# Optimization experiments

Hardware: AMD Instinct MI355X
Metric: run time of the kernel (lower is better)

Reference implementation:

```python
import jax, jax.numpy as jnp
import numpy as np

H = 1024        # hidden_dim
MD = 2048       # memory_dim
L = 16384       # memory length == max_length
N = 8           # head_N
# sys.float_info.min underflows to 0.0 in float32, exactly as in the torch
# original (python float * float32 tensor). Kept for faithfulness.
TINY = jnp.float32(2.2250738585072014e-308)


def setup_inputs() -> dict:
    key = jax.random.key(0)
    ks = jax.random.split(key, 12)
    s_h = 1.0 / np.sqrt(H)
    s_m = 1.0 / np.sqrt(MD)
    s_o = 1.0 / np.sqrt(2 * H)
    return {
        "x": jax.random.normal(ks[0], (1, 1, H), jnp.float32),
        "memory": jax.random.normal(ks[1], (L, MD), jnp.float32),
        "Wq": jax.random.uniform(ks[2], (H, H), jnp.float32, -s_h, s_h),
        "bq": jax.random.uniform(ks[3], (H,), jnp.float32, -s_h, s_h),
        "Wk": jax.random.uniform(ks[4], (H, MD), jnp.float32, -s_m, s_m),
        "bk": jax.random.uniform(ks[5], (H,), jnp.float32, -s_m, s_m),
        "Wv": jax.random.uniform(ks[6], (H, MD), jnp.float32, -s_m, s_m),
        "bv": jax.random.uniform(ks[7], (H,), jnp.float32, -s_m, s_m),
        "Wo": jax.random.uniform(ks[8], (H, 2 * H), jnp.float32, -s_o, s_o),
        "bo": jax.random.uniform(ks[9], (H,), jnp.float32, -s_o, s_o),
    }


def reference(x, memory, Wq, bq, Wk, bk, Wv, bv, Wo, bo):
    d = H // N  # per-head dim
    # Q: (1,H) -> (1,d,N) -> (N,1,d), scaled by d**-0.5
    q = x.reshape(1, -1) @ Wq.T + bq
    Q = q.reshape(1, d, N).transpose(2, 0, 1) * (d ** -0.5)
    # K: (L,H) -> (L,d,N) -> (N,d,L)
    K = (memory @ Wk.T + bk).reshape(-1, d, N).transpose(2, 1, 0)
    QK = jnp.einsum('nod,ndl->nol', Q, K)  # (N,1,L)
    # pad mask: 1 where the memory row sums to zero, else 0 (as in torch nonzero-set)
    any_zero = memory.sum(axis=1)
    pad_mask = (any_zero == 0).astype(QK.dtype)[None, None, :]
    QK = QK + pad_mask * TINY
    attn = jax.nn.softmax(QK, axis=-1)
    # V: (L,H) -> (L,d,N) -> (N,L,d)
    V = (memory @ Wv.T + bv).reshape(-1, d, N).transpose(2, 0, 1)
    feat = jnp.einsum('nol,nld->nod', attn, V)      # (N,1,d)
    feat = feat.transpose(1, 2, 0).reshape(1, 1, H)  # (1,1,H)
    ax = jnp.concatenate([x, feat], axis=-1)         # (1,1,2H)
    return jax.nn.relu(ax @ Wo.T + bo)
```

## Files before the change

### kernel.cpp

```cpp
#include <hip/hip_runtime.h>
#include <math.h>

#define HDIM  1024
#define MDIM  2048
#define RSQRT_D 0.08838834764831844f

#define OFF_W     0
#define OFF_BETA  16384
#define OFF_Z     16392
#define OFF_Q     16400
#define OFF_FEAT  17424
#define OFF_Y     18448
#define OFF_ZP    34832
#define OFF_BAR   38928
#define OFF_YBUF  301072

__device__ __forceinline__ float dot4(float4 a, float4 b) {
  return a.x * b.x + a.y * b.y + a.z * b.z + a.w * b.w;
}
__device__ __forceinline__ void fma4(float4& acc, float s, float4 v) {
  acc.x = fmaf(s, v.x, acc.x); acc.y = fmaf(s, v.y, acc.y);
  acc.z = fmaf(s, v.z, acc.z); acc.w = fmaf(s, v.w, acc.w);
}
__device__ __forceinline__ void add4(float4& a, float4 v) {
  a.x += v.x; a.y += v.y; a.z += v.z; a.w += v.w;
}

__device__ __forceinline__ void kbar(unsigned* ctr, int tid) {
  __syncthreads();
  if (tid == 0) {
    __hip_atomic_fetch_add(ctr, 1u, __ATOMIC_ACQ_REL, __HIP_MEMORY_SCOPE_AGENT);
    while (__hip_atomic_load(ctr, __ATOMIC_RELAXED, __HIP_MEMORY_SCOPE_AGENT) < 256u)
      __builtin_amdgcn_s_sleep(8);
    (void)__hip_atomic_load(ctr, __ATOMIC_ACQUIRE, __HIP_MEMORY_SCOPE_AGENT);
  }
  __syncthreads();
}

__global__ __launch_bounds__(256) void kq(const float* __restrict__ x,
                                          const float* __restrict__ Wq,
                                          const float* __restrict__ bq,
                                          float* __restrict__ ws) {
  int tid = threadIdx.x, lane = tid & 63;
  int j = blockIdx.x * 4 + (tid >> 6);
  const float4* xr = (const float4*)x;
  const float4* wr = (const float4*)(Wq + (size_t)j * HDIM);
  float acc = 0.f;
#pragma unroll
  for (int i = 0; i < 4; ++i) {
    int idx = i * 64 + lane;
    acc += dot4(xr[idx], wr[idx]);
  }
#pragma unroll
  for (int off = 32; off; off >>= 1) acc += __shfl_xor(acc, off);
  if (lane == 0) ws[OFF_Q + j] = acc + bq[j];
  if (tid < 64) ws[OFF_W + blockIdx.x * 64 + tid] = 0.f;
}

__global__ __launch_bounds__(256) void kw(const float* __restrict__ Wk,
                                          const float* __restrict__ bk,
                                          float* __restrict__ ws) {
  __shared__ float lds[32];
  int tid = threadIdx.x;
  const float* q = ws + OFF_Q;
  if (blockIdx.x == 256) {
    float b = 0.f;
#pragma unroll
    for (int i = 0; i < 4; ++i) {
      int c = tid + 256 * i;
      b = fmaf(q[c], bk[c], b);
    }
    b += __shfl_xor(b, 8); b += __shfl_xor(b, 16); b += __shfl_xor(b, 32);
    if ((tid & 63) < 8) lds[(tid >> 6) * 8 + (tid & 7)] = b;
    __syncthreads();
    if (tid < 8)
      ws[OFF_BETA + tid] = lds[tid] + lds[8 + tid] + lds[16 + tid] + lds[24 + tid];
    return;
  }
  int mc = blockIdx.x & 7, cc = blockIdx.x >> 3;
  int m = mc * 256 + tid;
  float acc[8];
#pragma unroll
  for (int n = 0; n < 8; ++n) acc[n] = 0.f;
  int c0 = cc * 32;
#pragma unroll
  for (int cb = 0; cb < 32; cb += 8) {
#pragma unroll
    for (int u = 0; u < 8; ++u)
      acc[u] = fmaf(q[c0 + cb + u], Wk[(size_t)(c0 + cb + u) * MDIM + m], acc[u]);
  }
#pragma unroll
  for (int n = 0; n < 8; ++n) atomicAdd(&ws[OFF_W + n * MDIM + m], acc[n]);
}

__global__ __launch_bounds__(512, 4) void kab(const float* __restrict__ mem,
                                              float* __restrict__ ws) {
  __shared__ float4 wlds[4096];
  __shared__ __align__(16) float pp[256];
  __shared__ float zz[64];
  __shared__ float bb[8];
  int tid = threadIdx.x, lane = tid & 63, wv = tid >> 6;
  int bid = blockIdx.x;
  int r0 = bid * 32;

  if (bid == 0 && tid < 2) ((unsigned*)(ws + OFF_BAR))[tid] = 0u;

  const float4* wsrc = (const float4*)(ws + OFF_W);
#pragma unroll
  for (int k = 0; k < 8; ++k)
    wlds[k * 512 + tid] = wsrc[k * 512 + tid];
  if (tid < 8) bb[tid] = ws[OFF_BETA + tid];

  const float* rowp = mem + (size_t)(r0 + wv * 4) * MDIM;
  float4 mva[4], mvan[4], mvb[4];
#pragma unroll
  for (int i = 0; i < 4; ++i)
    mva[i] = *(const float4*)(rowp + (i * 64 + lane) * 4);
  __syncthreads();

  float zacc[8];
#pragma unroll
  for (int n = 0; n < 8; ++n) zacc[n] = 0.f;

#pragma unroll
  for (int rl = 0; rl < 4; ++rl) {
#pragma unroll
    for (int i = 0; i < 4; ++i)
      mvb[i] = *(const float4*)(rowp + 1024 + (i * 64 + lane) * 4);
    float acc[8];
#pragma unroll
    for (int n = 0; n < 8; ++n) acc[n] = 0.f;
#pragma unroll
    for (int pass = 0; pass < 4; ++pass) {
      int cq = pass * 64 + lane;
#pragma unroll
      for (int n = 0; n < 8; ++n) {
        float4 w4 = wlds[n * 512 + cq];
        acc[n] = fmaf(mva[pass].x, w4.x, acc[n]);
        acc[n] = fmaf(mva[pass].y, w4.y, acc[n]);
        acc[n] = fmaf(mva[pass].z, w4.z, acc[n]);
        acc[n] = fmaf(mva[pass].w, w4.w, acc[n]);
      }
    }
    if (rl < 3) {
#pragma unroll
      for (int i = 0; i < 4; ++i)
        mvan[i] = *(const float4*)(rowp + MDIM + (i * 64 + lane) * 4);
    }
#pragma unroll
    for (int pass = 0; pass < 4; ++pass) {
      int cq = 256 + pass * 64 + lane;
#pragma unroll
      for (int n = 0; n < 8; ++n) {
        float4 w4 = wlds[n * 512 + cq];
        acc[n] = fmaf(mvb[pass].x, w4.x, acc[n]);
        acc[n] = fmaf(mvb[pass].y, w4.y, acc[n]);
        acc[n] = fmaf(mvb[pass].z, w4.z, acc[n]);
        acc[n] = fmaf(mvb[pass].w, w4.w, acc[n]);
      }
    }
#pragma unroll
    for (int off = 1; off < 64; off <<= 1)
#pragma unroll
      for (int n = 0; n < 8; ++n)
        acc[n] += __shfl_xor(acc[n], off);
#pragma unroll
    for (int n = 0; n < 8; ++n) {
      float p = __expf((acc[n] + bb[n]) * RSQRT_D);
      zacc[n] += p;
      if (lane == 0) pp[(wv * 4 + rl) * 8 + n] = p;
    }
#pragma unroll
    for (int i = 0; i < 4; ++i) mva[i] = mvan[i];
    rowp += MDIM;
  }
  if (lane == 0) {
#pragma unroll
    for (int n = 0; n < 8; ++n) zz[wv * 8 + n] = zacc[n];
  }
  __syncthreads();
  if (tid < 8) {
    float z = 0.f;
#pragma unroll
    for (int w = 0; w < 8; ++w) z += zz[w * 8 + tid];
    ws[OFF_ZP + bid * 8 + tid] = z;
  }

  float4 acc4[8];
#pragma unroll
  for (int n = 0; n < 8; ++n) acc4[n] = make_float4(0.f, 0.f, 0.f, 0.f);
  const float* base = mem + (size_t)r0 * MDIM + tid * 4;
  const float4* pp4 = (const float4*)pp;
#pragma unroll 4
  for (int r = 0; r < 32; ++r) {
    float4 mv = *(const float4*)(base + (size_t)r * MDIM);
    float4 pA = pp4[r * 2], pB = pp4[r * 2 + 1];
    fma4(acc4[0], pA.x, mv); fma4(acc4[1], pA.y, mv);
    fma4(acc4[2], pA.z, mv); fma4(acc4[3], pA.w, mv);
    fma4(acc4[4], pB.x, mv); fma4(acc4[5], pB.y, mv);
    fma4(acc4[6], pB.z, mv); fma4(acc4[7], pB.w, mv);
  }
  float* yb = ws + OFF_YBUF + (size_t)bid * 16384 + tid * 4;
#pragma unroll
  for (int n = 0; n < 8; ++n)
    *(float4*)(yb + n * MDIM) = acc4[n];
}

__global__ __launch_bounds__(256) void kyfo(const float* __restrict__ x,
                                            const float* __restrict__ Wv,
                                            const float* __restrict__ bv,
                                            const float* __restrict__ Wo,
                                            const float* __restrict__ bo,
                                            float* __restrict__ ws,
                                            float* __restrict__ out) {
  __shared__ __align__(16) float lds[1056];
  int tid = threadIdx.x, lane = tid & 63, wv = tid >> 6;
  int bid = blockIdx.x;

  {
    float4* sA = (float4*)lds;
    int quad = bid * 16 + (tid & 15);
    int b0 = (tid >> 4) * 32;
    const float4* src = (const float4*)(ws + OFF_YBUF);
    float4 acc = make_float4(0.f, 0.f, 0.f, 0.f);
    for (int b = b0; b < b0 + 32; ++b)
      add4(acc, src[(size_t)b * 4096 + quad]);
    sA[(tid & 15) * 16 + (tid >> 4)] = acc;
    __syncthreads();
    if (tid < 16) {
      float4 s = sA[tid * 16];
#pragma unroll
      for (int j = 1; j < 16; ++j) add4(s, sA[tid * 16 + j]);
      ((float4*)(ws + OFF_Y))[bid * 16 + tid] = s;
    }
  }
  if (bid == 0) {
    int n = tid & 7;
    float z = 0.f;
#pragma unroll
    for (int i = 0; i < 16; ++i)
      z += ws[OFF_ZP + ((tid >> 3) + 32 * i) * 8 + n];
    z += __shfl_xor(z, 8); z += __shfl_xor(z, 16); z += __shfl_xor(z, 32);
    float* zzz = lds + 1024;
    if (lane < 8) zzz[wv * 8 + lane] = z;
    __syncthreads();
    if (tid < 8)
      ws[OFF_Z + tid] = zzz[tid] + zzz[8 + tid] + zzz[16 + tid] + zzz[24 + tid];
  }
  kbar((unsigned*)(ws + OFF_BAR), tid);

  {
    int c = bid * 4 + wv;
    int n = c & 7;
    const float4* yb = (const float4*)(ws + OFF_Y + n * MDIM);
    const float4* wb = (const float4*)(Wv + (size_t)c * MDIM);
    float acc = 0.f;
#pragma unroll
    for (int s = 0; s < 8; ++s) {
      int idx = s * 64 + lane;
      acc += dot4(yb[idx], wb[idx]);
    }
#pragma unroll
    for (int off = 32; off; off >>= 1) acc += __shfl_xor(acc, off);
    if (lane == 0) ws[OFF_FEAT + c] = acc / ws[OFF_Z + n] + bv[c];
  }
  kbar((unsigned*)(ws + OFF_BAR) + 1, tid);

  {
    int j = bid * 4 + wv;
    const float4* wb = (const float4*)(Wo + (size_t)j * 2048);
    const float4* xr = (const float4*)x;
    const float4* fr = (const float4*)(ws + OFF_FEAT);
    float acc = 0.f;
#pragma unroll
    for (int s = 0; s < 4; ++s) {
      int idx = s * 64 + lane;
      acc += dot4(xr[idx], wb[idx]);
      acc += dot4(fr[idx], wb[256 + idx]);
    }
#pragma unroll
    for (int off = 32; off; off >>= 1) acc += __shfl_xor(acc, off);
    if (lane == 0) out[j] = fmaxf(acc + bo[j], 0.f);
  }
}

extern "C" void kernel_launch(void* const* d_in, const int* in_sizes, int n_in,
                              void* d_out, int out_size, void* d_ws, size_t ws_size,
                              hipStream_t stream) {
  const float* x   = (const float*)d_in[0];
  const float* mem = (const float*)d_in[1];
  const float* Wq  = (const float*)d_in[2];
  const float* bq  = (const float*)d_in[3];
  const float* Wk  = (const float*)d_in[4];
  const float* bk  = (const float*)d_in[5];
  const float* Wv  = (const float*)d_in[6];
  const float* bv  = (const float*)d_in[7];
  const float* Wo  = (const float*)d_in[8];
  const float* bo  = (const float*)d_in[9];
  float* ws  = (float*)d_ws;
  float* out = (float*)d_out;

  kq  <<<256, 256, 0, stream>>>(x, Wq, bq, ws);
  kw  <<<257, 256, 0, stream>>>(Wk, bk, ws);
  kab <<<512, 512, 0, stream>>>(mem, ws);
  kyfo<<<256, 256, 0, stream>>>(x, Wv, bv, Wo, bo, ws, out);
}
```

Measured before the change: 281.5 us.

## Fuse all stages into one persistent kernel with hierarchical grid barriers

Replaces the four separate launches with a single 256-block, 1024-thread persistent kernel. Stage boundaries become two-level grid barriers: 16 groups of 16 blocks, each group counter padded to its own cache line, then a root counter. Barrier counters are zeroed by a memset before the launch. Each block now handles 64 memory rows, and the partial-sum buffer reduction is reworked with wave shuffles. The aim is to remove launch gaps and cut barrier atomic contention, at the cost of relying on all 256 blocks being co-resident and on more idle waves in the small GEMV phases.

```diff
diff --git a/kernel.cpp b/kernel.cpp
--- a/kernel.cpp
+++ b/kernel.cpp
@@ -5,15 +5,15 @@
 #define MDIM  2048
 #define RSQRT_D 0.08838834764831844f
 
-#define OFF_W     0
-#define OFF_BETA  16384
-#define OFF_Z     16392
-#define OFF_Q     16400
-#define OFF_FEAT  17424
-#define OFF_Y     18448
-#define OFF_ZP    34832
-#define OFF_BAR   38928
-#define OFF_YBUF  301072
+#define OFF_BAR   0
+#define OFF_W     4096
+#define OFF_BETA  20480
+#define OFF_Z     20488
+#define OFF_Q     20496
+#define OFF_FEAT  21520
+#define OFF_Y     22544
+#define OFF_ZP    38928
+#define OFF_YBUF  41984
 
 __device__ __forceinline__ float dot4(float4 a, float4 b) {
   return a.x * b.x + a.y * b.y + a.z * b.z + a.w * b.w;
@@ -26,261 +26,266 @@
   a.x += v.x; a.y += v.y; a.z += v.z; a.w += v.w;
 }
 
-__device__ __forceinline__ void kbar(unsigned* ctr, int tid) {
+__device__ __forceinline__ void gbar(unsigned* bar, int k, int bid, int tid) {
   __syncthreads();
   if (tid == 0) {
-    __hip_atomic_fetch_add(ctr, 1u, __ATOMIC_ACQ_REL, __HIP_MEMORY_SCOPE_AGENT);
-    while (__hip_atomic_load(ctr, __ATOMIC_RELAXED, __HIP_MEMORY_SCOPE_AGENT) < 256u)
-      __builtin_amdgcn_s_sleep(8);
-    (void)__hip_atomic_load(ctr, __ATOMIC_ACQUIRE, __HIP_MEMORY_SCOPE_AGENT);
+    unsigned* grp  = bar + (size_t)k * 17 * 32;
+    unsigned* root = grp + 16 * 32;
+    unsigned r = __hip_atomic_fetch_add(&grp[(bid & 15) * 32], 1u,
+                                        __ATOMIC_ACQ_REL, __HIP_MEMORY_SCOPE_AGENT);
+    if (r == 15u)
+      __hip_atomic_fetch_add(root, 1u, __ATOMIC_ACQ_REL, __HIP_MEMORY_SCOPE_AGENT);
+    while (__hip_atomic_load(root, __ATOMIC_RELAXED, __HIP_MEMORY_SCOPE_AGENT) < 16u)
+      __builtin_amdgcn_s_sleep(1);
+    (void)__hip_atomic_load(root, __ATOMIC_ACQUIRE, __HIP_MEMORY_SCOPE_AGENT);
   }
   __syncthreads();
 }
 
-__global__ __launch_bounds__(256) void kq(const float* __restrict__ x,
-                                          const float* __restrict__ Wq,
-                                          const float* __restrict__ bq,
-                                          float* __restrict__ ws) {
-  int tid = threadIdx.x, lane = tid & 63;
-  int j = blockIdx.x * 4 + (tid >> 6);
-  const float4* xr = (const float4*)x;
-  const float4* wr = (const float4*)(Wq + (size_t)j * HDIM);
-  float acc = 0.f;
-#pragma unroll
-  for (int i = 0; i < 4; ++i) {
-    int idx = i * 64 + lane;
-    acc += dot4(xr[idx], wr[idx]);
-  }
-#pragma unroll
-  for (int off = 32; off; off >>= 1) acc += __shfl_xor(acc, off);
-  if (lane == 0) ws[OFF_Q + j] = acc + bq[j];
-  if (tid < 64) ws[OFF_W + blockIdx.x * 64 + tid] = 0.f;
-}
-
-__global__ __launch_bounds__(256) void kw(const float* __restrict__ Wk,
-                                          const float* __restrict__ bk,
-                                          float* __restrict__ ws) {
-  __shared__ float lds[32];
-  int tid = threadIdx.x;
-  const float* q = ws + OFF_Q;
-  if (blockIdx.x == 256) {
-    float b = 0.f;
+__global__ __launch_bounds__(1024, 4) void fused(const float* __restrict__ x,
+                                                 const float* __restrict__ mem,
+                                                 const float* __restrict__ Wq,
+                                                 const float* __restrict__ bq,
+                                                 const float* __restrict__ Wk,
+                                                 const float* __restrict__ bk,
+                                                 const float* __restrict__ Wv,
+                                                 const float* __restrict__ bv,
+                                                 const float* __restrict__ Wo,
+                                                 const float* __restrict__ bo,
+                                                 float* __restrict__ ws,
+                                                 float* __restrict__ out) {
+  __shared__ __align__(16) float4 lbuf[4260];
+  unsigned* bar = (unsigned*)ws;
+  int tid = threadIdx.x, lane = tid & 63, wv = tid >> 6;
+  int bid = blockIdx.x;
+
+  if (wv < 4) {
+    int j = bid * 4 + wv;
+    const float4* xr = (const float4*)x;
+    const float4* wr = (const float4*)(Wq + (size_t)j * HDIM);
+    float a = 0.f;
 #pragma unroll
     for (int i = 0; i < 4; ++i) {
-      int c = tid + 256 * i;
-      b = fmaf(q[c], bk[c], b);
-    }
-    b += __shfl_xor(b, 8); b += __shfl_xor(b, 16); b += __shfl_xor(b, 32);
-    if ((tid & 63) < 8) lds[(tid >> 6) * 8 + (tid & 7)] = b;
+      int idx = i * 64 + lane;
+      a += dot4(xr[idx], wr[idx]);
+    }
+#pragma unroll
+    for (int off = 32; off; off >>= 1) a += __shfl_xor(a, off);
+    if (lane == 0) ws[OFF_Q + j] = a + bq[j];
+  }
+  if (tid < 64) ws[OFF_W + bid * 64 + tid] = 0.f;
+  gbar(bar, 0, bid, tid);
+
+  if (bid < 128) {
+    int mc = bid & 3, cc = bid >> 2;
+    int m = mc * 512 + (tid & 511);
+    int c0 = cc * 32 + (tid >> 9) * 16;
+    const float* q = ws + OFF_Q;
+    float acc[8];
+#pragma unroll
+    for (int n = 0; n < 8; ++n) acc[n] = 0.f;
+#pragma unroll
+    for (int cb = 0; cb < 16; cb += 8)
+#pragma unroll
+      for (int u = 0; u < 8; ++u)
+        acc[u] = fmaf(q[c0 + cb + u], Wk[(size_t)(c0 + cb + u) * MDIM + m], acc[u]);
+#pragma unroll
+    for (int n = 0; n < 8; ++n) atomicAdd(&ws[OFF_W + n * MDIM + m], acc[n]);
+  } else if (bid == 255) {
+    float* bl = (float*)lbuf;
+    if (tid < 256) {
+      float b = 0.f;
+#pragma unroll
+      for (int i = 0; i < 4; ++i) {
+        int c = tid + 256 * i;
+        b = fmaf(ws[OFF_Q + c], bk[c], b);
+      }
+      b += __shfl_xor(b, 8); b += __shfl_xor(b, 16); b += __shfl_xor(b, 32);
+      if (lane < 8) bl[wv * 8 + lane] = b;
+    }
     __syncthreads();
     if (tid < 8)
-      ws[OFF_BETA + tid] = lds[tid] + lds[8 + tid] + lds[16 + tid] + lds[24 + tid];
-    return;
-  }
-  int mc = blockIdx.x & 7, cc = blockIdx.x >> 3;
-  int m = mc * 256 + tid;
-  float acc[8];
-#pragma unroll
-  for (int n = 0; n < 8; ++n) acc[n] = 0.f;
-  int c0 = cc * 32;
-#pragma unroll
-  for (int cb = 0; cb < 32; cb += 8) {
-#pragma unroll
-    for (int u = 0; u < 8; ++u)
-      acc[u] = fmaf(q[c0 + cb + u], Wk[(size_t)(c0 + cb + u) * MDIM + m], acc[u]);
-  }
-#pragma unroll
-  for (int n = 0; n < 8; ++n) atomicAdd(&ws[OFF_W + n * MDIM + m], acc[n]);
-}
-
-__global__ __launch_bounds__(512, 4) void kab(const float* __restrict__ mem,
-                                              float* __restrict__ ws) {
-  __shared__ float4 wlds[4096];
-  __shared__ __align__(16) float pp[256];
-  __shared__ float zz[64];
-  __shared__ float bb[8];
-  int tid = threadIdx.x, lane = tid & 63, wv = tid >> 6;
-  int bid = blockIdx.x;
-  int r0 = bid * 32;
-
-  if (bid == 0 && tid < 2) ((unsigned*)(ws + OFF_BAR))[tid] = 0u;
-
-  const float4* wsrc = (const float4*)(ws + OFF_W);
-#pragma unroll
-  for (int k = 0; k < 8; ++k)
-    wlds[k * 512 + tid] = wsrc[k * 512 + tid];
-  if (tid < 8) bb[tid] = ws[OFF_BETA + tid];
-
-  const float* rowp = mem + (size_t)(r0 + wv * 4) * MDIM;
-  float4 mva[4], mvan[4], mvb[4];
-#pragma unroll
-  for (int i = 0; i < 4; ++i)
-    mva[i] = *(const float4*)(rowp + (i * 64 + lane) * 4);
-  __syncthreads();
-
-  float zacc[8];
-#pragma unroll
-  for (int n = 0; n < 8; ++n) zacc[n] = 0.f;
-
-#pragma unroll
-  for (int rl = 0; rl < 4; ++rl) {
+      ws[OFF_BETA + tid] = bl[tid] + bl[8 + tid] + bl[16 + tid] + bl[24 + tid];
+  }
+  gbar(bar, 1, bid, tid);
+
+  {
+    float4* wlds = lbuf;
+    float* pp = (float*)(lbuf + 4096);
+    float* zz = pp + 512;
+    float* bb = zz + 128;
+    const float4* wsrc = (const float4*)(ws + OFF_W);
+#pragma unroll
+    for (int k = 0; k < 4; ++k)
+      wlds[k * 1024 + tid] = wsrc[k * 1024 + tid];
+    if (tid < 8) bb[tid] = ws[OFF_BETA + tid];
+
+    int r0b = bid * 64;
+    const float* rowp = mem + (size_t)(r0b + wv * 4) * MDIM;
+    float4 mva[4], mvan[4], mvb[4];
 #pragma unroll
     for (int i = 0; i < 4; ++i)
-      mvb[i] = *(const float4*)(rowp + 1024 + (i * 64 + lane) * 4);
-    float acc[8];
-#pragma unroll
-    for (int n = 0; n < 8; ++n) acc[n] = 0.f;
-#pragma unroll
-    for (int pass = 0; pass < 4; ++pass) {
-      int cq = pass * 64 + lane;
+      mva[i] = *(const float4*)(rowp + (i * 64 + lane) * 4);
+    __syncthreads();
+
+    float zacc[8];
+#pragma unroll
+    for (int n = 0; n < 8; ++n) zacc[n] = 0.f;
+
+#pragma unroll
+    for (int rl = 0; rl < 4; ++rl) {
+#pragma unroll
+      for (int i = 0; i < 4; ++i)
+        mvb[i] = *(const float4*)(rowp + 1024 + (i * 64 + lane) * 4);
+      float acc[8];
+#pragma unroll
+      for (int n = 0; n < 8; ++n) acc[n] = 0.f;
+#pragma unroll
+      for (int pass = 0; pass < 4; ++pass) {
+        int cq = pass * 64 + lane;
+#pragma unroll
+        for (int n = 0; n < 8; ++n) {
+          float4 w4 = wlds[n * 512 + cq];
+          acc[n] = fmaf(mva[pass].x, w4.x, acc[n]);
+          acc[n] = fmaf(mva[pass].y, w4.y, acc[n]);
+          acc[n] = fmaf(mva[pass].z, w4.z, acc[n]);
+          acc[n] = fmaf(mva[pass].w, w4.w, acc[n]);
+        }
+      }
+      if (rl < 3) {
+#pragma unroll
+        for (int i = 0; i < 4; ++i)
+          mvan[i] = *(const float4*)(rowp + MDIM + (i * 64 + lane) * 4);
+      }
+#pragma unroll
+      for (int pass = 0; pass < 4; ++pass) {
+        int cq = 256 + pass * 64 + lane;
+#pragma unroll
+        for (int n = 0; n < 8; ++n) {
+          float4 w4 = wlds[n * 512 + cq];
+          acc[n] = fmaf(mvb[pass].x, w4.x, acc[n]);
+          acc[n] = fmaf(mvb[pass].y, w4.y, acc[n]);
+          acc[n] = fmaf(mvb[pass].z, w4.z, acc[n]);
+          acc[n] = fmaf(mvb[pass].w, w4.w, acc[n]);
+        }
+      }
+#pragma unroll
+      for (int off = 1; off < 64; off <<= 1)
+#pragma unroll
+        for (int n = 0; n < 8; ++n)
+          acc[n] += __shfl_xor(acc[n], off);
 #pragma unroll
       for (int n = 0; n < 8; ++n) {
-        float4 w4 = wlds[n * 512 + cq];
-        acc[n] = fmaf(mva[pass].x, w4.x, acc[n]);
-        acc[n] = fmaf(mva[pass].y, w4.y, acc[n]);
-        acc[n] = fmaf(mva[pass].z, w4.z, acc[n]);
-        acc[n] = fmaf(mva[pass].w, w4.w, acc[n]);
-      }
-    }
-    if (rl < 3) {
-#pragma unroll
-      for (int i = 0; i < 4; ++i)
-        mvan[i] = *(const float4*)(rowp + MDIM + (i * 64 + lane) * 4);
-    }
-#pragma unroll
-    for (int pass = 0; pass < 4; ++pass) {
-      int cq = 256 + pass * 64 + lane;
-#pragma unroll
-      for (int n = 0; n < 8; ++n) {
-        float4 w4 = wlds[n * 512 + cq];
-        acc[n] = fmaf(mvb[pass].x, w4.x, acc[n]);
-        acc[n] = fmaf(mvb[pass].y, w4.y, acc[n]);
-        acc[n] = fmaf(mvb[pass].z, w4.z, acc[n]);
-        acc[n] = fmaf(mvb[pass].w, w4.w, acc[n]);
-      }
-    }
-#pragma unroll
-    for (int off = 1; off < 64; off <<= 1)
-#pragma unroll
-      for (int n = 0; n < 8; ++n)
-        acc[n] += __shfl_xor(acc[n], off);
-#pragma unroll
-    for (int n = 0; n < 8; ++n) {
-      float p = __expf((acc[n] + bb[n]) * RSQRT_D);
-      zacc[n] += p;
-      if (lane == 0) pp[(wv * 4 + rl) * 8 + n] = p;
-    }
-#pragma unroll
-    for (int i = 0; i < 4; ++i) mva[i] = mvan[i];
-    rowp += MDIM;
-  }
-  if (lane == 0) {
-#pragma unroll
-    for (int n = 0; n < 8; ++n) zz[wv * 8 + n] = zacc[n];
-  }
-  __syncthreads();
-  if (tid < 8) {
-    float z = 0.f;
-#pragma unroll
-    for (int w = 0; w < 8; ++w) z += zz[w * 8 + tid];
-    ws[OFF_ZP + bid * 8 + tid] = z;
-  }
-
-  float4 acc4[8];
-#pragma unroll
-  for (int n = 0; n < 8; ++n) acc4[n] = make_float4(0.f, 0.f, 0.f, 0.f);
-  const float* base = mem + (size_t)r0 * MDIM + tid * 4;
-  const float4* pp4 = (const float4*)pp;
+        float p = __expf((acc[n] + bb[n]) * RSQRT_D);
+        zacc[n] += p;
+        if (lane == 0) pp[(wv * 4 + rl) * 8 + n] = p;
+      }
+#pragma unroll
+      for (int i = 0; i < 4; ++i) mva[i] = mvan[i];
+      rowp += MDIM;
+    }
+    if (lane == 0) {
+#pragma unroll
+      for (int n = 0; n < 8; ++n) zz[wv * 8 + n] = zacc[n];
+    }
+    __syncthreads();
+    if (tid < 8) {
+      float z = 0.f;
+#pragma unroll
+      for (int w = 0; w < 16; ++w) z += zz[w * 8 + tid];
+      ws[OFF_ZP + bid * 8 + tid] = z;
+    }
+    int h = tid >> 9, t5 = tid & 511;
+    float4 acc4[8];
+#pragma unroll
+    for (int n = 0; n < 8; ++n) acc4[n] = make_float4(0.f, 0.f, 0.f, 0.f);
+    const float* base = mem + (size_t)(r0b + h * 32) * MDIM + t5 * 4;
+    const float4* pp4 = (const float4*)pp + h * 64;
 #pragma unroll 4
-  for (int r = 0; r < 32; ++r) {
-    float4 mv = *(const float4*)(base + (size_t)r * MDIM);
-    float4 pA = pp4[r * 2], pB = pp4[r * 2 + 1];
-    fma4(acc4[0], pA.x, mv); fma4(acc4[1], pA.y, mv);
-    fma4(acc4[2], pA.z, mv); fma4(acc4[3], pA.w, mv);
-    fma4(acc4[4], pB.x, mv); fma4(acc4[5], pB.y, mv);
-    fma4(acc4[6], pB.z, mv); fma4(acc4[7], pB.w, mv);
-  }
-  float* yb = ws + OFF_YBUF + (size_t)bid * 16384 + tid * 4;
-#pragma unroll
-  for (int n = 0; n < 8; ++n)
-    *(float4*)(yb + n * MDIM) = acc4[n];
-}
-
-__global__ __launch_bounds__(256) void kyfo(const float* __restrict__ x,
-                                            const float* __restrict__ Wv,
-                                            const float* __restrict__ bv,
-                                            const float* __restrict__ Wo,
-                                            const float* __restrict__ bo,
-                                            float* __restrict__ ws,
-                                            float* __restrict__ out) {
-  __shared__ __align__(16) float lds[1056];
-  int tid = threadIdx.x, lane = tid & 63, wv = tid >> 6;
-  int bid = blockIdx.x;
+    for (int r = 0; r < 32; ++r) {
+      float4 mv = *(const float4*)(base + (size_t)r * MDIM);
+      float4 pA = pp4[r * 2], pB = pp4[r * 2 + 1];
+      fma4(acc4[0], pA.x, mv); fma4(acc4[1], pA.y, mv);
+      fma4(acc4[2], pA.z, mv); fma4(acc4[3], pA.w, mv);
+      fma4(acc4[4], pB.x, mv); fma4(acc4[5], pB.y, mv);
+      fma4(acc4[6], pB.z, mv); fma4(acc4[7], pB.w, mv);
+    }
+    float* yb = ws + OFF_YBUF + (size_t)(bid * 2 + h) * 16384 + t5 * 4;
+#pragma unroll
+    for (int n = 0; n < 8; ++n)
+      *(float4*)(yb + n * MDIM) = acc4[n];
+  }
+  gbar(bar, 2, bid, tid);
 
   {
-    float4* sA = (float4*)lds;
-    int quad = bid * 16 + (tid & 15);
-    int b0 = (tid >> 4) * 32;
+    float4* sA = lbuf;
+    int ql = tid & 15, h64 = tid >> 4;
+    int quad = bid * 16 + ql;
     const float4* src = (const float4*)(ws + OFF_YBUF);
-    float4 acc = make_float4(0.f, 0.f, 0.f, 0.f);
-    for (int b = b0; b < b0 + 32; ++b)
-      add4(acc, src[(size_t)b * 4096 + quad]);
-    sA[(tid & 15) * 16 + (tid >> 4)] = acc;
+    float4 a = make_float4(0.f, 0.f, 0.f, 0.f);
+#pragma unroll
+    for (int i = 0; i < 8; ++i)
+      add4(a, src[(size_t)(h64 + 64 * i) * 4096 + quad]);
+    sA[ql * 64 + h64] = a;
     __syncthreads();
-    if (tid < 16) {
-      float4 s = sA[tid * 16];
-#pragma unroll
-      for (int j = 1; j < 16; ++j) add4(s, sA[tid * 16 + j]);
-      ((float4*)(ws + OFF_Y))[bid * 16 + tid] = s;
-    }
-  }
-  if (bid == 0) {
-    int n = tid & 7;
-    float z = 0.f;
-#pragma unroll
-    for (int i = 0; i < 16; ++i)
-      z += ws[OFF_ZP + ((tid >> 3) + 32 * i) * 8 + n];
-    z += __shfl_xor(z, 8); z += __shfl_xor(z, 16); z += __shfl_xor(z, 32);
-    float* zzz = lds + 1024;
-    if (lane < 8) zzz[wv * 8 + lane] = z;
-    __syncthreads();
-    if (tid < 8)
-      ws[OFF_Z + tid] = zzz[tid] + zzz[8 + tid] + zzz[16 + tid] + zzz[24 + tid];
-  }
-  kbar((unsigned*)(ws + OFF_BAR), tid);
-
-  {
-    int c = bid * 4 + wv;
-    int n = c & 7;
-    const float4* yb = (const float4*)(ws + OFF_Y + n * MDIM);
-    const float4* wb = (const float4*)(Wv + (size_t)c * MDIM);
-    float acc = 0.f;
+    float4 v = sA[wv * 64 + lane];
+#pragma unroll
+    for (int off = 1; off < 64; off <<= 1) {
+      v.x += __shfl_xor(v.x, off);
+      v.y += __shfl_xor(v.y, off);
+      v.z += __shfl_xor(v.z, off);
+      v.w += __shfl_xor(v.w, off);
+    }
+    if (lane == 0) ((float4*)(ws + OFF_Y))[bid * 16 + wv] = v;
+    if (bid == 0) {
+      float* zzz = (float*)(lbuf + 2048);
+      if (tid < 256) {
+        int n = tid & 7;
+        float z = 0.f;
+#pragma unroll
+        for (int i = 0; i < 8; ++i)
+          z += ws[OFF_ZP + ((tid >> 3) + 32 * i) * 8 + n];
+        z += __shfl_xor(z, 8); z += __shfl_xor(z, 16); z += __shfl_xor(z, 32);
+        if (lane < 8) zzz[wv * 8 + lane] = z;
+      }
+      __syncthreads();
+      if (tid < 8)
+        ws[OFF_Z + tid] = zzz[tid] + zzz[8 + tid] + zzz[16 + tid] + zzz[24 + tid];
+    }
+  }
+  gbar(bar, 3, bid, tid);
+
+  if (wv < 4) {
+    int c = bid * 4 + wv, n = c & 7;
+    const float4* yb4 = (const float4*)(ws + OFF_Y + n * MDIM);
+    const float4* wb4 = (const float4*)(Wv + (size_t)c * MDIM);
+    float a = 0.f;
 #pragma unroll
     for (int s = 0; s < 8; ++s) {
       int idx = s * 64 + lane;
-      acc += dot4(yb[idx], wb[idx]);
-    }
-#pragma unroll
-    for (int off = 32; off; off >>= 1) acc += __shfl_xor(acc, off);
-    if (lane == 0) ws[OFF_FEAT + c] = acc / ws[OFF_Z + n] + bv[c];
-  }
-  kbar((unsigned*)(ws + OFF_BAR) + 1, tid);
-
-  {
+      a += dot4(yb4[idx], wb4[idx]);
+    }
+#pragma unroll
+    for (int off = 32; off; off >>= 1) a += __shfl_xor(a, off);
+    if (lane == 0) ws[OFF_FEAT + c] = a / ws[OFF_Z + n] + bv[c];
+  }
+  gbar(bar, 4, bid, tid);
+
+  if (wv < 4) {
     int j = bid * 4 + wv;
     const float4* wb = (const float4*)(Wo + (size_t)j * 2048);
     const float4* xr = (const float4*)x;
     const float4* fr = (const float4*)(ws + OFF_FEAT);
-    float acc = 0.f;
+    float a = 0.f;
 #pragma unroll
     for (int s = 0; s < 4; ++s) {
       int idx = s * 64 + lane;
-      acc += dot4(xr[idx], wb[idx]);
-      acc += dot4(fr[idx], wb[256 + idx]);
-    }
-#pragma unroll
-    for (int off = 32; off; off >>= 1) acc += __shfl_xor(acc, off);
-    if (lane == 0) out[j] = fmaxf(acc + bo[j], 0.f);
+      a += dot4(xr[idx], wb[idx]);
+      a += dot4(fr[idx], wb[256 + idx]);
+    }
+#pragma unroll
+    for (int off = 32; off; off >>= 1) a += __shfl_xor(a, off);
+    if (lane == 0) out[j] = fmaxf(a + bo[j], 0.f);
   }
 }
 
@@ -300,8 +305,7 @@
   float* ws  = (float*)d_ws;
   float* out = (float*)d_out;
 
-  kq  <<<256, 256, 0, stream>>>(x, Wq, bq, ws);
-  kw  <<<257, 256, 0, stream>>>(Wk, bk, ws);
-  kab <<<512, 512, 0, stream>>>(mem, ws);
-  kyfo<<<256, 256, 0, stream>>>(x, Wv, bv, Wo, bo, ws, out);
-}
+  hipMemsetAsync(ws, 0, 6 * 17 * 32 * 4, stream);
+
+  fused<<<256, 1024, 0, stream>>>(x, mem, Wq, bq, Wk, bk, Wv, bv, Wo, bo, ws, out);
+}
```

Result: slower. 308.3 us (+9.5%).

## Use hierarchical grid barrier and wider blocks for final reduction kernel

Applied to the files above, without the earlier changes.

Replaces the flat single-counter grid barrier with a two-level barrier: 16 padded group counters feed a root counter, and the spin uses a shorter sleep. All barrier counters are now zeroed in the first kernel. The final kernel runs 1024 threads per block so the partial-sum reduction over the 512 per-block Y buffers has more parallelism, using shuffle reductions. The YBUF offset moves closer to the other workspace data. Only 4 of 16 waves take part in the Wv and Wo GEMV phases, and the barrier adds an extra atomic hop.

```diff
diff --git a/kernel.cpp b/kernel.cpp
--- a/kernel.cpp
+++ b/kernel.cpp
@@ -13,7 +13,7 @@
 #define OFF_Y     18448
 #define OFF_ZP    34832
 #define OFF_BAR   38928
-#define OFF_YBUF  301072
+#define OFF_YBUF  41984
 
 __device__ __forceinline__ float dot4(float4 a, float4 b) {
   return a.x * b.x + a.y * b.y + a.z * b.z + a.w * b.w;
@@ -26,13 +26,18 @@
   a.x += v.x; a.y += v.y; a.z += v.z; a.w += v.w;
 }
 
-__device__ __forceinline__ void kbar(unsigned* ctr, int tid) {
+__device__ __forceinline__ void gbar(unsigned* bar, int k, int bid, int tid) {
   __syncthreads();
   if (tid == 0) {
-    __hip_atomic_fetch_add(ctr, 1u, __ATOMIC_ACQ_REL, __HIP_MEMORY_SCOPE_AGENT);
-    while (__hip_atomic_load(ctr, __ATOMIC_RELAXED, __HIP_MEMORY_SCOPE_AGENT) < 256u)
-      __builtin_amdgcn_s_sleep(8);
-    (void)__hip_atomic_load(ctr, __ATOMIC_ACQUIRE, __HIP_MEMORY_SCOPE_AGENT);
+    unsigned* grp  = bar + (size_t)k * 17 * 32;
+    unsigned* root = grp + 16 * 32;
+    unsigned r = __hip_atomic_fetch_add(&grp[(bid & 15) * 32], 1u,
+                                        __ATOMIC_ACQ_REL, __HIP_MEMORY_SCOPE_AGENT);
+    if (r == 15u)
+      __hip_atomic_fetch_add(root, 1u, __ATOMIC_ACQ_REL, __HIP_MEMORY_SCOPE_AGENT);
+    while (__hip_atomic_load(root, __ATOMIC_RELAXED, __HIP_MEMORY_SCOPE_AGENT) < 16u)
+      __builtin_amdgcn_s_sleep(1);
+    (void)__hip_atomic_load(root, __ATOMIC_ACQUIRE, __HIP_MEMORY_SCOPE_AGENT);
   }
   __syncthreads();
 }
@@ -55,6 +60,8 @@
   for (int off = 32; off; off >>= 1) acc += __shfl_xor(acc, off);
   if (lane == 0) ws[OFF_Q + j] = acc + bq[j];
   if (tid < 64) ws[OFF_W + blockIdx.x * 64 + tid] = 0.f;
+  int z = blockIdx.x * 256 + tid;
+  if (z < 1088) ((unsigned*)(ws + OFF_BAR))[z] = 0u;
 }
 
 __global__ __launch_bounds__(256) void kw(const float* __restrict__ Wk,
@@ -102,8 +109,6 @@
   int tid = threadIdx.x, lane = tid & 63, wv = tid >> 6;
   int bid = blockIdx.x;
   int r0 = bid * 32;
-
-  if (bid == 0 && tid < 2) ((unsigned*)(ws + OFF_BAR))[tid] = 0u;
 
   const float4* wsrc = (const float4*)(ws + OFF_W);
 #pragma unroll
@@ -206,81 +211,86 @@
     *(float4*)(yb + n * MDIM) = acc4[n];
 }
 
-__global__ __launch_bounds__(256) void kyfo(const float* __restrict__ x,
-                                            const float* __restrict__ Wv,
-                                            const float* __restrict__ bv,
-                                            const float* __restrict__ Wo,
-                                            const float* __restrict__ bo,
-                                            float* __restrict__ ws,
-                                            float* __restrict__ out) {
-  __shared__ __align__(16) float lds[1056];
+__global__ __launch_bounds__(1024, 4) void kyfo2(const float* __restrict__ x,
+                                                 const float* __restrict__ Wv,
+                                                 const float* __restrict__ bv,
+                                                 const float* __restrict__ Wo,
+                                                 const float* __restrict__ bo,
+                                                 float* __restrict__ ws,
+                                                 float* __restrict__ out) {
+  __shared__ __align__(16) float4 sA[1040];
+  __shared__ float zzz[32];
+  unsigned* bar = (unsigned*)(ws + OFF_BAR);
   int tid = threadIdx.x, lane = tid & 63, wv = tid >> 6;
   int bid = blockIdx.x;
 
   {
-    float4* sA = (float4*)lds;
-    int quad = bid * 16 + (tid & 15);
-    int b0 = (tid >> 4) * 32;
+    int ql = tid & 15, h64 = tid >> 4;
+    int quad = bid * 16 + ql;
     const float4* src = (const float4*)(ws + OFF_YBUF);
-    float4 acc = make_float4(0.f, 0.f, 0.f, 0.f);
-    for (int b = b0; b < b0 + 32; ++b)
-      add4(acc, src[(size_t)b * 4096 + quad]);
-    sA[(tid & 15) * 16 + (tid >> 4)] = acc;
+    float4 a = make_float4(0.f, 0.f, 0.f, 0.f);
+#pragma unroll
+    for (int i = 0; i < 8; ++i)
+      add4(a, src[(size_t)(h64 + 64 * i) * 4096 + quad]);
+    sA[ql * 65 + h64] = a;
     __syncthreads();
-    if (tid < 16) {
-      float4 s = sA[tid * 16];
-#pragma unroll
-      for (int j = 1; j < 16; ++j) add4(s, sA[tid * 16 + j]);
-      ((float4*)(ws + OFF_Y))[bid * 16 + tid] = s;
-    }
+    float4 v = sA[wv * 65 + lane];
+#pragma unroll
+    for (int off = 1; off < 64; off <<= 1) {
+      v.x += __shfl_xor(v.x, off);
+      v.y += __shfl_xor(v.y, off);
+      v.z += __shfl_xor(v.z, off);
+      v.w += __shfl_xor(v.w, off);
+    }
+    if (lane == 0) ((float4*)(ws + OFF_Y))[bid * 16 + wv] = v;
   }
   if (bid == 0) {
-    int n = tid & 7;
-    float z = 0.f;
-#pragma unroll
-    for (int i = 0; i < 16; ++i)
-      z += ws[OFF_ZP + ((tid >> 3) + 32 * i) * 8 + n];
-    z += __shfl_xor(z, 8); z += __shfl_xor(z, 16); z += __shfl_xor(z, 32);
-    float* zzz = lds + 1024;
-    if (lane < 8) zzz[wv * 8 + lane] = z;
+    if (tid < 256) {
+      int n = tid & 7;
+      float z = 0.f;
+#pragma unroll
+      for (int i = 0; i < 16; ++i)
+        z += ws[OFF_ZP + ((tid >> 3) + 32 * i) * 8 + n];
+      z += __shfl_xor(z, 8); z += __shfl_xor(z, 16); z += __shfl_xor(z, 32);
+      if (lane < 8) zzz[(tid >> 6) * 8 + lane] = z;
+    }
     __syncthreads();
     if (tid < 8)
       ws[OFF_Z + tid] = zzz[tid] + zzz[8 + tid] + zzz[16 + tid] + zzz[24 + tid];
   }
-  kbar((unsigned*)(ws + OFF_BAR), tid);
-
-  {
-    int c = bid * 4 + wv;
-    int n = c & 7;
-    const float4* yb = (const float4*)(ws + OFF_Y + n * MDIM);
-    const float4* wb = (const float4*)(Wv + (size_t)c * MDIM);
-    float acc = 0.f;
+  gbar(bar, 0, bid, tid);
+
+  if (wv < 4) {
+    int c = bid * 4 + wv, n = c & 7;
+    const float4* yb4 = (const float4*)(ws + OFF_Y + n * MDIM);
+    const float4* wb4 = (const float4*)(Wv + (size_t)c * MDIM);
+    float a = 0.f;
 #pragma unroll
     for (int s = 0; s < 8; ++s) {
       int idx = s * 64 + lane;
-      acc += dot4(yb[idx], wb[idx]);
-    }
-#pragma unroll
-    for (int off = 32; off; off >>= 1) acc += __shfl_xor(acc, off);
-    if (lane == 0) ws[OFF_FEAT + c] = acc / ws[OFF_Z + n] + bv[c];
-  }
-  kbar((unsigned*)(ws + OFF_BAR) + 1, tid);
-
-  {
+      a += dot4(yb4[idx], wb4[idx]);
+    }
+#pragma unroll
+    for (int off = 32; off; off >>= 1) a += __shfl_xor(a, off);
+    if (lane == 0) ws[OFF_FEAT + c] = a / ws[OFF_Z + n] + bv[c];
+  }
+  gbar(bar, 1, bid, tid);
+
+  if (wv < 4) {
     int j = bid * 4 + wv;
     const float4* wb = (const float4*)(Wo + (size_t)j * 2048);
     const float4* xr = (const float4*)x;
     const float4* fr = (const float4*)(ws + OFF_FEAT);
-    float acc = 0.f;
+    float a = 0.f;
 #pragma unroll
     for (int s = 0; s < 4; ++s) {
       int idx = s * 64 + lane;
-      acc += dot4(xr[idx], wb[idx]);
-      acc += dot4(fr[idx], wb[256 + idx]);
-    }
-#pragma unroll
-    for (int off = 32; off; off >>= 1) acc += __shfl_xor(acc, off);
-    if (lane == 0) out[j] = fmaxf(acc + bo[j], 0.f);
+      a += dot4(xr[idx], wb[idx]);
+      a += dot4(fr[idx], wb[256 + idx]);
+    }
+#pragma unroll
+    for (int off = 32; off; off >>= 1) a += __shfl_xor(a, off);
+    if (lane == 0) out[j] = fmaxf(a + bo[j], 0.f);
   }
 }
 
@@ -300,8 +310,8 @@
   float* ws  = (float*)d_ws;
   float* out = (float*)d_out;
 
-  kq  <<<256, 256, 0, stream>>>(x, Wq, bq, ws);
-  kw  <<<257, 256, 0, stream>>>(Wk, bk, ws);
-  kab <<<512, 512, 0, stream>>>(mem, ws);
-  kyfo<<<256, 256, 0, stream>>>(x, Wv, bv, Wo, bo, ws, out);
-}
+  kq   <<<256, 256,  0, stream>>>(x, Wq, bq, ws);
+  kw   <<<257, 256,  0, stream>>>(Wk, bk, ws);
+  kab  <<<512, 512,  0, stream>>>(mem, ws);
+  kyfo2<<<256, 1024, 0, stream>>>(x, Wv, bv, Wo, bo, ws, out);
+}
```

Result: faster. 273.3 us (-2.9%).
